# Kernel optimization log

Hardware: AMD Instinct MI355X
Metric: run time of the kernel (lower is better)

## Reference

```python
import jax, jax.numpy as jnp
import numpy as np

N_NODES = 50000
N_EDGES = 800000
F_IN, C1, C2 = 128, 100, 4
NEG_SLOPE = 0.2  # PyG GATConv default LeakyReLU slope


def setup_inputs() -> dict:
    key = jax.random.key(0)
    ks = jax.random.split(key, 10)
    def glorot(k, shape):
        fan = sum(shape)
        return jax.random.normal(k, shape, jnp.float32) * jnp.sqrt(2.0 / fan)
    return {
        "x": jax.random.normal(ks[0], (N_NODES, F_IN), jnp.float32),
        "edge_index": jax.random.randint(ks[1], (2, N_EDGES), 0, N_NODES, jnp.int64),
        "W1": glorot(ks[2], (F_IN, C1)),
        "att_src1": glorot(ks[3], (1, C1)),
        "att_dst1": glorot(ks[4], (1, C1)),
        "b1": jnp.zeros((C1,), jnp.float32),
        "W2": glorot(ks[5], (C1, C2)),
        "att_src2": glorot(ks[6], (1, C2)),
        "att_dst2": glorot(ks[7], (1, C2)),
        "b2": jnp.zeros((C2,), jnp.float32),
    }


def _gat_conv(x, edge_index, W, att_src, att_dst, bias):
    """PyG GATConv (heads=1, concat=True, add_self_loops=True), eval mode."""
    n = x.shape[0]
    # add self loops
    loop = jnp.arange(n, dtype=edge_index.dtype)
    src = jnp.concatenate([edge_index[0], loop])
    dst = jnp.concatenate([edge_index[1], loop])
    h = x @ W                                   # [N, C]
    a_src = (h * att_src[0]).sum(-1)            # [N]
    a_dst = (h * att_dst[0]).sum(-1)            # [N]
    e = jax.nn.leaky_relu(a_src[src] + a_dst[dst], NEG_SLOPE)  # [E+N]
    # segment softmax over destination neighborhoods
    m = jax.ops.segment_max(e, dst, num_segments=n)            # [N]
    w = jnp.exp(e - m[dst])
    denom = jax.ops.segment_sum(w, dst, num_segments=n)        # [N]
    alpha = w / denom[dst]                                     # [E+N]
    msg = h[src] * alpha[:, None]                              # [E+N, C]
    out = jax.ops.segment_sum(msg, dst, num_segments=n)        # [N, C]
    return out + bias


def reference(x, edge_index, W1, att_src1, att_dst1, b1, W2, att_src2, att_dst2, b2):
    h = _gat_conv(x, edge_index, W1, att_src1, att_dst1, b1)
    h = jax.nn.relu(h)  # dropout is identity in eval mode
    h = _gat_conv(h, edge_index, W2, att_src2, att_dst2, b2)
    return jax.nn.log_softmax(h, axis=1)
```

## Files before the change

### kernel.cpp

```cpp
#include <hip/hip_runtime.h>
#include <math.h>

#define N_NODES 50000
#define N_EDGES 800000
#define F_IN 128
#define C1 100
#define C1D 50
#define C2 4
#define NEG 0.2f
#define NB_ZERO 196
#define NB_E4 782
#define DEGCAP 64
#define CSTR 16

typedef __attribute__((ext_vector_type(8))) short bf16x8;
typedef __attribute__((ext_vector_type(4))) float f32x4;

__device__ __forceinline__ float leaky(float v) { return v > 0.f ? v : NEG * v; }
__device__ __forceinline__ unsigned f2bf(float f) {
    unsigned u = __float_as_uint(f);
    u += 0x7FFF + ((u >> 16) & 1);
    return u >> 16;
}
__device__ __forceinline__ float bf_lo(unsigned g) { return __uint_as_float(g << 16); }
__device__ __forceinline__ float bf_hi(unsigned g) { return __uint_as_float(g & 0xFFFF0000u); }

__global__ __launch_bounds__(256) void k_prep(int* __restrict__ cnt, const float* __restrict__ W1,
                                              unsigned short* __restrict__ W1bf) {
    int i = blockIdx.x * 256 + threadIdx.x;
    if (i < N_NODES) cnt[i * CSTR] = 0;
    if (i < 12800) {
        int k = i / 100, n = i - k * 100;
        W1bf[n * 128 + k] = (unsigned short)f2bf(W1[i]);
    } else if (i < 12800 + 12 * 128) {
        int e = i - 12800;
        int n = 100 + (e >> 7), k = e & 127;
        W1bf[n * 128 + k] = 0;
    }
}

__global__ __attribute__((amdgpu_waves_per_eu(1, 3))) __launch_bounds__(256)
void k_gemm_scatter(const float* __restrict__ x, const unsigned short* __restrict__ W1bf,
                    const float* __restrict__ as1, const float* __restrict__ ad1,
                    unsigned* __restrict__ h1b, float* __restrict__ a_src1,
                    float* __restrict__ a_dst1, const int* __restrict__ ei,
                    int* __restrict__ cnt, unsigned short* __restrict__ slots) {
    int half = blockIdx.x >> 1;
    if (blockIdx.x & 1) {
        int i = half * 256 + threadIdx.x;
        if (i >= N_EDGES / 4) return;
        int4 s4 = *(const int4*)(ei + i * 4);
        int4 d4 = *(const int4*)(ei + N_EDGES + i * 4);
        int sl;
        sl = atomicAdd(&cnt[d4.x * CSTR], 1); if (sl < DEGCAP) slots[d4.x * DEGCAP + sl] = (unsigned short)s4.x;
        sl = atomicAdd(&cnt[d4.y * CSTR], 1); if (sl < DEGCAP) slots[d4.y * DEGCAP + sl] = (unsigned short)s4.y;
        sl = atomicAdd(&cnt[d4.z * CSTR], 1); if (sl < DEGCAP) slots[d4.z * DEGCAP + sl] = (unsigned short)s4.z;
        sl = atomicAdd(&cnt[d4.w * CSTR], 1); if (sl < DEGCAP) slots[d4.w * DEGCAP + sl] = (unsigned short)s4.w;
        return;
    }
    int tid = threadIdx.x;
    int node0 = half * 64;
    int wave = tid >> 6, lane = tid & 63;
    int mrow = lane & 15;
    int quad = lane >> 4;
    int na = node0 + wave * 16 + mrow;
    bool vrow = na < N_NODES;
    const float* px = x + (long)na * F_IN + quad * 8;

    bf16x8 afr[4];
#pragma unroll
    for (int kc = 0; kc < 4; ++kc) {
        float4 v0 = make_float4(0.f, 0.f, 0.f, 0.f), v1 = v0;
        if (vrow) {
            v0 = *(const float4*)(px + kc * 32);
            v1 = *(const float4*)(px + kc * 32 + 4);
        }
        bf16x8 t;
        t[0] = (short)f2bf(v0.x); t[1] = (short)f2bf(v0.y);
        t[2] = (short)f2bf(v0.z); t[3] = (short)f2bf(v0.w);
        t[4] = (short)f2bf(v1.x); t[5] = (short)f2bf(v1.y);
        t[6] = (short)f2bf(v1.z); t[7] = (short)f2bf(v1.w);
        afr[kc] = t;
    }

    f32x4 acc[7];
#pragma unroll
    for (int nt = 0; nt < 7; ++nt) {
        const unsigned short* pb = W1bf + (nt * 16 + mrow) * 128 + quad * 8;
        f32x4 a = {0.f, 0.f, 0.f, 0.f};
#pragma unroll
        for (int kc = 0; kc < 4; ++kc) {
            bf16x8 bfr = *(const bf16x8*)(pb + kc * 32);
            a = __builtin_amdgcn_mfma_f32_16x16x32_bf16(afr[kc], bfr, a, 0, 0, 0);
        }
        acc[nt] = a;
    }

    float ps[4] = {0.f, 0.f, 0.f, 0.f}, pd[4] = {0.f, 0.f, 0.f, 0.f};
#pragma unroll
    for (int nt = 0; nt < 7; ++nt) {
        int col = nt * 16 + mrow;
        float av = 0.f, dv = 0.f;
        if (col < C1) { av = as1[col]; dv = ad1[col]; }
#pragma unroll
        for (int r = 0; r < 4; ++r) {
            ps[r] += acc[nt][r] * av;
            pd[r] += acc[nt][r] * dv;
        }
    }
#pragma unroll
    for (int r = 0; r < 4; ++r) {
#pragma unroll
        for (int off = 1; off < 16; off <<= 1) {
            ps[r] += __shfl_xor(ps[r], off);
            pd[r] += __shfl_xor(pd[r], off);
        }
    }
    if (mrow == 0) {
#pragma unroll
        for (int r = 0; r < 4; ++r) {
            int n = node0 + wave * 16 + quad * 4 + r;
            if (n < N_NODES) { a_src1[n] = ps[r]; a_dst1[n] = pd[r]; }
        }
    }

#pragma unroll
    for (int nt = 0; nt < 7; ++nt) {
#pragma unroll
        for (int r = 0; r < 4; ++r) {
            float v = acc[nt][r];
            float o = __shfl_xor(v, 1);
            int col = nt * 16 + mrow;
            int n = node0 + wave * 16 + quad * 4 + r;
            if ((mrow & 1) == 0 && col < C1 && n < N_NODES) {
                unsigned pk = f2bf(v) | (f2bf(o) << 16);
                h1b[(long)n * C1D + (col >> 1)] = pk;
            }
        }
    }
}

__device__ __forceinline__ float rlanef(float v, int l) {
    return __int_as_float(__builtin_amdgcn_readlane(__float_as_int(v), l));
}

__global__ __launch_bounds__(256) void k_agg1(const unsigned* __restrict__ h1b, const float* __restrict__ a_src,
                                              const float* __restrict__ a_dst, const int* __restrict__ cnt,
                                              const unsigned short* __restrict__ slots, const float* __restrict__ b1,
                                              const float* __restrict__ W2, const float* __restrict__ as2,
                                              const float* __restrict__ ad2, float4* __restrict__ h2,
                                              float* __restrict__ a_src2, float* __restrict__ a_dst2) {
    __shared__ float sW2[C1 * C2];
    __shared__ float sB1[C1];
    int tid = threadIdx.x;
    for (int f = tid; f < C1 * C2; f += 256) sW2[f] = W2[f];
    if (tid < C1) sB1[tid] = b1[tid];
    __syncthreads();
    int wave = tid >> 6, lane = tid & 63;
    int d = blockIdx.x * 4 + wave;
    if (d >= N_NODES) return;
    int cn = min(cnt[d * CSTR], DEGCAP);
    float ad = a_dst[d];
    int c = lane;
    bool act = c < C1D;

    float wself = __expf(leaky(a_src[d] + ad));
    unsigned gs = act ? h1b[(long)d * C1D + c] : 0u;
    float accL = wself * bf_lo(gs), accH = wself * bf_hi(gs);
    float lsum = (lane == 0) ? wself : 0.f;

    int sreg = 0; float wreg = 0.f;
    if (lane < cn) {
        sreg = (int)slots[d * DEGCAP + lane];
        wreg = __expf(leaky(a_src[sreg] + ad));
        lsum += wreg;
    }

    unsigned ga[8], gb[8];
#define LD(buf, e) { int sv_ = __builtin_amdgcn_readlane(sreg, (e)); \
                     buf = act ? h1b[(long)sv_ * C1D + c] : 0u; }
#define CONSUME(buf, e) if ((e) < cn) { float w_ = rlanef(wreg, (e)); \
                     accL += w_ * bf_lo(buf); accH += w_ * bf_hi(buf); }

#pragma unroll
    for (int i = 0; i < 8; ++i) LD(ga[i], i);
#pragma unroll
    for (int bp = 0; bp < 4; ++bp) {
        const int b0 = 2 * bp, b1 = 2 * bp + 1;
        if (b0 * 8 >= cn) break;
        if (b1 * 8 < cn) {
#pragma unroll
            for (int i = 0; i < 8; ++i) LD(gb[i], b1 * 8 + i);
        }
#pragma unroll
        for (int i = 0; i < 8; ++i) CONSUME(ga[i], b0 * 8 + i);
        if (b1 * 8 >= cn) break;
        if ((b1 + 1) * 8 < cn) {
#pragma unroll
            for (int i = 0; i < 8; ++i) LD(ga[i], (b1 + 1) * 8 + i);
        }
#pragma unroll
        for (int i = 0; i < 8; ++i) CONSUME(gb[i], b1 * 8 + i);
    }
#undef LD
#undef CONSUME

    for (int off = 32; off; off >>= 1) lsum += __shfl_xor(lsum, off);
    float invl = 1.f / lsum;
    float p0 = 0.f, p1 = 0.f, p2 = 0.f, p3 = 0.f;
    if (act) {
        float v0 = fmaxf(accL * invl + sB1[2 * c], 0.f);
        float v1 = fmaxf(accH * invl + sB1[2 * c + 1], 0.f);
        const float* w0 = &sW2[(2 * c) * 4];
        p0 = v0 * w0[0] + v1 * w0[4];
        p1 = v0 * w0[1] + v1 * w0[5];
        p2 = v0 * w0[2] + v1 * w0[6];
        p3 = v0 * w0[3] + v1 * w0[7];
    }
    for (int off = 32; off; off >>= 1) {
        p0 += __shfl_xor(p0, off);
        p1 += __shfl_xor(p1, off);
        p2 += __shfl_xor(p2, off);
        p3 += __shfl_xor(p3, off);
    }
    if (lane == 0) {
        h2[d] = make_float4(p0, p1, p2, p3);
        a_src2[d] = p0 * as2[0] + p1 * as2[1] + p2 * as2[2] + p3 * as2[3];
        a_dst2[d] = p0 * ad2[0] + p1 * ad2[1] + p2 * ad2[2] + p3 * ad2[3];
    }
}

__global__ __launch_bounds__(256) void k_agg2(const float4* __restrict__ h2, const float* __restrict__ a_src,
                                              const float* __restrict__ a_dst, const int* __restrict__ cnt,
                                              const unsigned short* __restrict__ slots, const float* __restrict__ b2,
                                              float4* __restrict__ out) {
    int wave = threadIdx.x >> 6, lane = threadIdx.x & 63;
    int grp = lane >> 4, li = lane & 15;
    int d = blockIdx.x * 16 + wave * 4 + grp;
    if (d >= N_NODES) return;
    int cn = min(cnt[d * CSTR], DEGCAP);
    float ad = a_dst[d];
    float l = 0.f, a0 = 0.f, a1 = 0.f, a2 = 0.f, a3 = 0.f;
    if (li == 0) {
        float w = __expf(leaky(a_src[d] + ad));
        float4 hv = h2[d];
        l = w; a0 = w * hv.x; a1 = w * hv.y; a2 = w * hv.z; a3 = w * hv.w;
    }
    for (int j = li; j < cn; j += 16) {
        int s = (int)slots[d * DEGCAP + j];
        float w = __expf(leaky(a_src[s] + ad));
        l += w;
        float4 hv = h2[s];
        a0 += w * hv.x; a1 += w * hv.y; a2 += w * hv.z; a3 += w * hv.w;
    }
#pragma unroll
    for (int off = 8; off; off >>= 1) {
        l += __shfl_xor(l, off);
        a0 += __shfl_xor(a0, off);
        a1 += __shfl_xor(a1, off);
        a2 += __shfl_xor(a2, off);
        a3 += __shfl_xor(a3, off);
    }
    if (li == 0) {
        float invl = 1.f / l;
        float v0 = a0 * invl + b2[0];
        float v1 = a1 * invl + b2[1];
        float v2 = a2 * invl + b2[2];
        float v3 = a3 * invl + b2[3];
        float mm = fmaxf(fmaxf(v0, v1), fmaxf(v2, v3));
        float ls = logf(__expf(v0 - mm) + __expf(v1 - mm) + __expf(v2 - mm) + __expf(v3 - mm)) + mm;
        out[d] = make_float4(v0 - ls, v1 - ls, v2 - ls, v3 - ls);
    }
}

extern "C" void kernel_launch(void* const* d_in, const int* in_sizes, int n_in,
                              void* d_out, int out_size, void* d_ws, size_t ws_size,
                              hipStream_t stream) {
    const float* x   = (const float*)d_in[0];
    const int*   ei  = (const int*)d_in[1];
    const float* W1  = (const float*)d_in[2];
    const float* as1 = (const float*)d_in[3];
    const float* ad1 = (const float*)d_in[4];
    const float* b1  = (const float*)d_in[5];
    const float* W2  = (const float*)d_in[6];
    const float* as2 = (const float*)d_in[7];
    const float* ad2 = (const float*)d_in[8];
    const float* b2  = (const float*)d_in[9];
    float4* out = (float4*)d_out;

    char* w = (char*)d_ws;
    unsigned* h1b    = (unsigned*)(w + 0);
    float*    a_src1 = (float*)(w + 10000000);
    float*    a_dst1 = (float*)(w + 10200000);
    float4*   h2     = (float4*)(w + 10400000);
    float*    a_src2 = (float*)(w + 11200000);
    float*    a_dst2 = (float*)(w + 11400000);
    int*      cnt    = (int*)(w + 11600000);
    unsigned short* slots = (unsigned short*)(w + 14800000);
    unsigned short* W1bf  = (unsigned short*)(w + 21200000);

    k_prep<<<NB_ZERO, 256, 0, stream>>>(cnt, W1, W1bf);
    k_gemm_scatter<<<2 * NB_E4, 256, 0, stream>>>(x, W1bf, as1, ad1, h1b, a_src1, a_dst1,
                                                  ei, cnt, slots);
    k_agg1<<<(N_NODES + 3) / 4, 256, 0, stream>>>(h1b, a_src1, a_dst1, cnt, slots, b1, W2, as2, ad2,
                                                  h2, a_src2, a_dst2);
    k_agg2<<<(N_NODES + 15) / 16, 256, 0, stream>>>(h2, a_src2, a_dst2, cnt, slots, b2, out);
}
```

Baseline: 173.2 us.

## Replace per-node global atomic scatter with two-pass bucketed CSR build

Replaces the per-edge global atomicAdd on padded per-node counters with a two-pass scheme. First, blocks bin edges into 196 coarse buckets of 256 destination nodes, using LDS atomics and one global atomic per bucket per block, and write packed (src,dst-low) records. Then a new k_bucket kernel builds per-node slot lists with LDS atomics and writes dense counts. This cuts contended global atomics and scattered writes, at the cost of an extra kernel launch, an intermediate buffer and fixed bucket-capacity truncation (BCAP).

```diff
diff --git a/kernel.cpp b/kernel.cpp
--- a/kernel.cpp
+++ b/kernel.cpp
@@ -8,10 +8,14 @@
 #define C1D 50
 #define C2 4
 #define NEG 0.2f
-#define NB_ZERO 196
-#define NB_E4 782
 #define DEGCAP 64
-#define CSTR 16
+#define NBUCK 196
+#define BCAP 4608
+#define BSTR 16
+#define PA_NB 196
+#define PA_CHUNK 1021
+#define GEMM_NB 782
+#define NB_PREP 56
 
 typedef __attribute__((ext_vector_type(8))) short bf16x8;
 typedef __attribute__((ext_vector_type(4))) float f32x4;
@@ -25,10 +29,10 @@
 __device__ __forceinline__ float bf_lo(unsigned g) { return __uint_as_float(g << 16); }
 __device__ __forceinline__ float bf_hi(unsigned g) { return __uint_as_float(g & 0xFFFF0000u); }
 
-__global__ __launch_bounds__(256) void k_prep(int* __restrict__ cnt, const float* __restrict__ W1,
+__global__ __launch_bounds__(256) void k_prep(int* __restrict__ bcnt, const float* __restrict__ W1,
                                               unsigned short* __restrict__ W1bf) {
     int i = blockIdx.x * 256 + threadIdx.x;
-    if (i < N_NODES) cnt[i * CSTR] = 0;
+    if (i < NBUCK) bcnt[i * BSTR] = 0;
     if (i < 12800) {
         int k = i / 100, n = i - k * 100;
         W1bf[n * 128 + k] = (unsigned short)f2bf(W1[i]);
@@ -44,20 +48,52 @@
                     const float* __restrict__ as1, const float* __restrict__ ad1,
                     unsigned* __restrict__ h1b, float* __restrict__ a_src1,
                     float* __restrict__ a_dst1, const int* __restrict__ ei,
-                    int* __restrict__ cnt, unsigned short* __restrict__ slots) {
-    int half = blockIdx.x >> 1;
-    if (blockIdx.x & 1) {
-        int i = half * 256 + threadIdx.x;
-        if (i >= N_EDGES / 4) return;
-        int4 s4 = *(const int4*)(ei + i * 4);
-        int4 d4 = *(const int4*)(ei + N_EDGES + i * 4);
-        int sl;
-        sl = atomicAdd(&cnt[d4.x * CSTR], 1); if (sl < DEGCAP) slots[d4.x * DEGCAP + sl] = (unsigned short)s4.x;
-        sl = atomicAdd(&cnt[d4.y * CSTR], 1); if (sl < DEGCAP) slots[d4.y * DEGCAP + sl] = (unsigned short)s4.y;
-        sl = atomicAdd(&cnt[d4.z * CSTR], 1); if (sl < DEGCAP) slots[d4.z * DEGCAP + sl] = (unsigned short)s4.z;
-        sl = atomicAdd(&cnt[d4.w * CSTR], 1); if (sl < DEGCAP) slots[d4.w * DEGCAP + sl] = (unsigned short)s4.w;
+                    int* __restrict__ bcnt, unsigned* __restrict__ breg) {
+    if (blockIdx.x < PA_NB) {
+        __shared__ int lcnt[NBUCK];
+        __shared__ int lbase[NBUCK];
+        int tid = threadIdx.x;
+        if (tid < NBUCK) lcnt[tid] = 0;
+        __syncthreads();
+        int g0 = blockIdx.x * PA_CHUNK;
+        int4 s4[4], d4[4];
+        int off[4][4];
+        bool val[4];
+#pragma unroll
+        for (int it = 0; it < 4; ++it) {
+            int local = it * 256 + tid;
+            int g = g0 + local;
+            val[it] = (local < PA_CHUNK) && (g < N_EDGES / 4);
+            if (val[it]) {
+                s4[it] = *(const int4*)(ei + (long)g * 4);
+                d4[it] = *(const int4*)(ei + N_EDGES + (long)g * 4);
+                off[it][0] = atomicAdd(&lcnt[d4[it].x >> 8], 1);
+                off[it][1] = atomicAdd(&lcnt[d4[it].y >> 8], 1);
+                off[it][2] = atomicAdd(&lcnt[d4[it].z >> 8], 1);
+                off[it][3] = atomicAdd(&lcnt[d4[it].w >> 8], 1);
+            }
+        }
+        __syncthreads();
+        if (tid < NBUCK) {
+            int c = lcnt[tid];
+            lbase[tid] = c ? atomicAdd(&bcnt[tid * BSTR], c) : 0;
+        }
+        __syncthreads();
+#pragma unroll
+        for (int it = 0; it < 4; ++it) {
+            if (!val[it]) continue;
+            { int b = d4[it].x >> 8; int p = lbase[b] + off[it][0];
+              if (p < BCAP) breg[b * BCAP + p] = ((unsigned)s4[it].x << 8) | ((unsigned)d4[it].x & 255u); }
+            { int b = d4[it].y >> 8; int p = lbase[b] + off[it][1];
+              if (p < BCAP) breg[b * BCAP + p] = ((unsigned)s4[it].y << 8) | ((unsigned)d4[it].y & 255u); }
+            { int b = d4[it].z >> 8; int p = lbase[b] + off[it][2];
+              if (p < BCAP) breg[b * BCAP + p] = ((unsigned)s4[it].z << 8) | ((unsigned)d4[it].z & 255u); }
+            { int b = d4[it].w >> 8; int p = lbase[b] + off[it][3];
+              if (p < BCAP) breg[b * BCAP + p] = ((unsigned)s4[it].w << 8) | ((unsigned)d4[it].w & 255u); }
+        }
         return;
     }
+    int half = blockIdx.x - PA_NB;
     int tid = threadIdx.x;
     int node0 = half * 64;
     int wave = tid >> 6, lane = tid & 63;
@@ -137,6 +173,29 @@
                 h1b[(long)n * C1D + (col >> 1)] = pk;
             }
         }
+    }
+}
+
+__global__ __launch_bounds__(512) void k_bucket(const unsigned* __restrict__ breg,
+                                                const int* __restrict__ bcnt,
+                                                int* __restrict__ cnt,
+                                                unsigned short* __restrict__ slots) {
+    __shared__ int dcnt[256];
+    int b = blockIdx.x, tid = threadIdx.x;
+    if (tid < 256) dcnt[tid] = 0;
+    __syncthreads();
+    int n = min(bcnt[b * BSTR], BCAP);
+    const unsigned* reg = breg + b * BCAP;
+    for (int e = tid; e < n; e += 512) {
+        unsigned p = reg[e];
+        int d8 = p & 255;
+        int slot = atomicAdd(&dcnt[d8], 1);
+        if (slot < DEGCAP) slots[(((b << 8) + d8) << 6) + slot] = (unsigned short)(p >> 8);
+    }
+    __syncthreads();
+    if (tid < 256) {
+        int d = (b << 8) + tid;
+        if (d < N_NODES) cnt[d] = dcnt[tid];
     }
 }
 
@@ -159,7 +218,7 @@
     int wave = tid >> 6, lane = tid & 63;
     int d = blockIdx.x * 4 + wave;
     if (d >= N_NODES) return;
-    int cn = min(cnt[d * CSTR], DEGCAP);
+    int cn = min(cnt[d], DEGCAP);
     float ad = a_dst[d];
     int c = lane;
     bool act = c < C1D;
@@ -238,7 +297,7 @@
     int grp = lane >> 4, li = lane & 15;
     int d = blockIdx.x * 16 + wave * 4 + grp;
     if (d >= N_NODES) return;
-    int cn = min(cnt[d * CSTR], DEGCAP);
+    int cn = min(cnt[d], DEGCAP);
     float ad = a_dst[d];
     float l = 0.f, a0 = 0.f, a1 = 0.f, a2 = 0.f, a3 = 0.f;
     if (li == 0) {
@@ -296,12 +355,15 @@
     float*    a_src2 = (float*)(w + 11200000);
     float*    a_dst2 = (float*)(w + 11400000);
     int*      cnt    = (int*)(w + 11600000);
-    unsigned short* slots = (unsigned short*)(w + 14800000);
-    unsigned short* W1bf  = (unsigned short*)(w + 21200000);
-
-    k_prep<<<NB_ZERO, 256, 0, stream>>>(cnt, W1, W1bf);
-    k_gemm_scatter<<<2 * NB_E4, 256, 0, stream>>>(x, W1bf, as1, ad1, h1b, a_src1, a_dst1,
-                                                  ei, cnt, slots);
+    int*      bcnt   = (int*)(w + 11800000);
+    unsigned short* slots = (unsigned short*)(w + 11816000);
+    unsigned* breg   = (unsigned*)(w + 18216000);
+    unsigned short* W1bf  = (unsigned short*)(w + 21828672);
+
+    k_prep<<<NB_PREP, 256, 0, stream>>>(bcnt, W1, W1bf);
+    k_gemm_scatter<<<PA_NB + GEMM_NB, 256, 0, stream>>>(x, W1bf, as1, ad1, h1b, a_src1, a_dst1,
+                                                        ei, bcnt, breg);
+    k_bucket<<<NBUCK, 512, 0, stream>>>(breg, bcnt, cnt, slots);
     k_agg1<<<(N_NODES + 3) / 4, 256, 0, stream>>>(h1b, a_src1, a_dst1, cnt, slots, b1, W2, as2, ad2,
                                                   h2, a_src2, a_dst2);
     k_agg2<<<(N_NODES + 15) / 16, 256, 0, stream>>>(h2, a_src2, a_dst2, cnt, slots, b2, out);
```

Result: faster. 165.4 us (-4.5%).
